# Kernel optimization log

Measured on AMD Instinct MI355X. Metric: run time of the kernel, lower is better.

Reference implementation:

```python
import jax, jax.numpy as jnp
import numpy as np

B, C, L = 4, 16, 1024
U_SELF, U_CROSS, HID = 32, 16, 128
WIDTH = 128
EPS = 1e-5
LN_EPS = 1e-14


def _band_mask(n, w):
    j = jnp.arange(n)
    lo = j - w // 2
    hi = lo + w
    i = j[:, None]
    return (lo <= i) & (i < hi)  # mask[i, j]: query i attends key j


def _layernorm(x, gamma, beta):
    # channel-first LN over dim 1; gamma/beta shape (C, 1)
    mean = jnp.mean(x, 1, keepdims=True)
    var = jnp.mean((x - mean) ** 2, 1, keepdims=True) + LN_EPS
    return (x - mean) / jnp.sqrt(var) * gamma + beta


def _self_attn(x, Wt, Wx, bh, Wa, ba):
    xt = x.transpose(0, 2, 1)                                # (B,L,C)
    q = xt @ Wt                                              # (B,L,U)
    k = xt @ Wx                                              # (B,L,U)
    h = jnp.tanh(q[:, :, None, :] + k[:, None, :, :] + bh)   # (B,L,L,U)
    e = jnp.squeeze(h @ Wa, -1) + ba                         # (B,L,L)
    e = jnp.exp(e - jnp.max(e, -1, keepdims=True))
    e = jnp.where(_band_mask(e.shape[1], WIDTH), e, 0.0)
    a = e / (jnp.sum(e, -1, keepdims=True) + EPS)
    v = a @ xt                                               # (B,L,C)
    return v.transpose(0, 2, 1)


def _ff(x, W1, b1, W2, b2):
    xt = x.transpose(0, 2, 1)
    h = jax.nn.relu(xt @ W1 + b1)
    return (h @ W2 + b2).transpose(0, 2, 1)


def _transformer(x, Wt, Wx, bh, Wa, ba, g1, be1, W1, b1, W2, b2, g2, be2):
    y = _layernorm(x + _self_attn(x, Wt, Wx, bh, Wa, ba), g1, be1)
    return _layernorm(y + _ff(y, W1, b1, W2, b2), g2, be2)


def _cross(y1, y2, Wq, Wk, Wv):
    y1t = y1.transpose(0, 2, 1)
    y2t = y2.transpose(0, 2, 1)
    q = y1t @ Wq
    k = y2t @ Wk
    v = y2t @ Wv                                             # (B,L,Uc)
    e = (q @ k.transpose(0, 2, 1)) * (1.0 / np.float32(np.sqrt(U_CROSS)))
    e = jnp.where(_band_mask(e.shape[-1], WIDTH), e, -jnp.inf)
    a = jax.nn.softmax(e, -1)
    return (a @ v).transpose(0, 2, 1)                        # (B,Uc,L)


def _forward(x1, x2, t1, t2, cw, top):
    y1 = _transformer(x1, *t1)
    y2 = _transformer(x2, *t2)
    g1, be1, W1, b1, W2, b2, g2, be2 = top
    y = _layernorm(y1 + _cross(y1, y2, *cw), g1, be1)
    return _layernorm(y + _ff(y, W1, b1, W2, b2), g2, be2)


def setup_inputs() -> dict:
    key = jax.random.key(0)
    ks = iter(jax.random.split(key, 64))
    u = lambda shape: jax.random.uniform(next(ks), shape, jnp.float32, -0.02, 0.02)
    n = lambda shape: jax.random.normal(next(ks), shape, jnp.float32) * 0.05
    d = {"x1": jax.random.normal(next(ks), (B, C, L), jnp.float32),
         "x2": jax.random.normal(next(ks), (B, C, L), jnp.float32)}
    for p in ("t1", "t2"):
        d[p + "_Wt"] = u((C, U_SELF)); d[p + "_Wx"] = u((C, U_SELF))
        d[p + "_bh"] = jnp.zeros(U_SELF)
        d[p + "_Wa"] = u((U_SELF, 1)); d[p + "_ba"] = jnp.zeros(1)
        d[p + "_g1"] = jnp.ones((C, 1)); d[p + "_be1"] = jnp.zeros((C, 1))
        d[p + "_W1"] = n((C, HID)); d[p + "_b1"] = jnp.zeros(HID)
        d[p + "_W2"] = n((HID, C)); d[p + "_b2"] = jnp.zeros(C)
        d[p + "_g2"] = jnp.ones((C, 1)); d[p + "_be2"] = jnp.zeros((C, 1))
    d["ca_Wq"] = u((C, U_CROSS)); d["ca_Wk"] = u((C, U_CROSS)); d["ca_Wv"] = u((C, U_CROSS))
    d["g1"] = jnp.ones((C, 1)); d["be1"] = jnp.zeros((C, 1))
    d["W1"] = n((C, HID)); d["b1"] = jnp.zeros(HID)
    d["W2"] = n((HID, C)); d["b2"] = jnp.zeros(C)
    d["g2"] = jnp.ones((C, 1)); d["be2"] = jnp.zeros((C, 1))
    return d


def reference(x1, x2, t1_Wt, t1_Wx, t1_bh, t1_Wa, t1_ba, t1_g1, t1_be1, t1_W1, t1_b1, t1_W2, t1_b2, t1_g2, t1_be2, t2_Wt, t2_Wx, t2_bh, t2_Wa, t2_ba, t2_g1, t2_be1, t2_W1, t2_b1, t2_W2, t2_b2, t2_g2, t2_be2, ca_Wq, ca_Wk, ca_Wv, g1, be1, W1, b1, W2, b2, g2, be2):
    t1 = (t1_Wt, t1_Wx, t1_bh, t1_Wa, t1_ba, t1_g1, t1_be1, t1_W1, t1_b1, t1_W2, t1_b2, t1_g2, t1_be2)
    t2 = (t2_Wt, t2_Wx, t2_bh, t2_Wa, t2_ba, t2_g1, t2_be1, t2_W1, t2_b1, t2_W2, t2_b2, t2_g2, t2_be2)
    cw = (ca_Wq, ca_Wk, ca_Wv)
    top = (g1, be1, W1, b1, W2, b2, g2, be2)
    return _forward(x1, x2, t1, t2, cw, top)
```

## Files before the change

### kernel.cpp

```cpp
#include <hip/hip_runtime.h>


#define L_    1024
#define C_    16
#define US_   32
#define HID_  128
#define TI1   8
#define TI2   4
#define K2    2.885390082f
#define L2E   1.442695041f

__device__ __forceinline__ float frcp(float x)  { return __builtin_amdgcn_rcpf(x); }
__device__ __forceinline__ float fexp2(float x) { return __builtin_amdgcn_exp2f(x); }

struct BranchP {
  const float *x, *Wt, *Wx, *bh, *Wa, *ba, *g1, *be1, *W1, *b1, *W2, *b2, *g2, *be2;
  float* y;
};

__global__ __launch_bounds__(256) void branch_kernel(BranchP Pa, BranchP Pb) {
  const BranchP P = blockIdx.z ? Pb : Pa;
  const int b   = blockIdx.y;
  const int i0  = blockIdx.x * TI1;
  const int tid = threadIdx.x;
  const int j0  = max(0, i0 - 63);
  const int j1  = min(L_, i0 + TI1 + 64);
  const int Wd  = j1 - j0;

  __shared__ float xs[C_][137];
  __shared__ union {
    struct { float ks[136][33]; float qs[TI1][33]; } a;
    struct { float W1s[C_][129]; float W2s[HID_][17]; float b1s[HID_]; } bb;
  } ovl;
  __shared__ float es[TI1][129];
  __shared__ float ya[TI1][17];
  __shared__ float Wts[C_][US_], Wxs[C_][US_];
  __shared__ float m2was[US_], bhs[US_];
  __shared__ float g1s[C_], be1s[C_], b2s[C_], g2s[C_], be2s[C_];
  __shared__ float bas;

  float w1r[8], w2r[8], b1r = 0.f;
#pragma unroll
  for (int t = 0; t < 8; ++t) { w1r[t] = P.W1[tid + 256 * t]; w2r[t] = P.W2[tid + 256 * t]; }
  if (tid < HID_) b1r = P.b1[tid];

  for (int idx = tid; idx < C_ * US_; idx += 256) {
    int c = idx >> 5, u = idx & 31;
    Wts[c][u] = K2 * P.Wt[idx];
    Wxs[c][u] = K2 * P.Wx[idx];
  }
  if (tid < US_) { m2was[tid] = -K2 * P.Wa[tid]; bhs[tid] = K2 * P.bh[tid]; }
  if (tid < C_) {
    g1s[tid] = P.g1[tid]; be1s[tid] = P.be1[tid];
    g2s[tid] = P.g2[tid]; be2s[tid] = P.be2[tid];
    b2s[tid] = P.b2[tid];
  }
  if (tid == 0) bas = P.ba[0];
  for (int idx = tid; idx < C_ * Wd; idx += 256) {
    int c = idx / Wd, jj = idx - c * Wd;
    xs[c][jj] = P.x[(b * C_ + c) * L_ + j0 + jj];
  }
  __syncthreads();

  for (int idx = tid; idx < Wd * US_; idx += 256) {
    int j = idx >> 5, u = idx & 31;
    float a = bhs[u];
#pragma unroll
    for (int c = 0; c < C_; ++c) a = fmaf(xs[c][j], Wxs[c][u], a);
    ovl.a.ks[j][u] = a;
  }
  {
    int i = tid >> 5, u = tid & 31;
    float a = 0.f;
#pragma unroll
    for (int c = 0; c < C_; ++c) a = fmaf(xs[c][i0 - j0 + i], Wts[c][u], a);
    ovl.a.qs[i][u] = a;
  }
  __syncthreads();

  const int il   = tid >> 5;
  const int sub  = tid & 31;
  const int ig   = i0 + il;
  const int jlo  = max(0, ig - 63), jhi = min(L_, ig + 65);
  const int nj   = jhi - jlo;
  const int jb   = jlo - j0;
  const int c16  = sub & 15;
  const int half = sub >> 4;

  float inv;
  {
    float xq[US_];
#pragma unroll
    for (int u = 0; u < US_; ++u) xq[u] = ovl.a.qs[il][u];
    float eacc = L2E * bas;
#pragma unroll
    for (int u = 0; u < US_; ++u) eacc -= 0.5f * m2was[u];
    float s = 0.f;
    for (int jj = sub; jj < nj; jj += 32) {
      const float* kr = ovl.a.ks[jb + jj];
      float acc = eacc;
#pragma unroll
      for (int u = 0; u < US_; ++u) {
        float t = fexp2(xq[u] + kr[u]);
        acc = fmaf(m2was[u], frcp(1.0f + t), acc);
      }
      float v = fexp2(acc);
      es[il][jj] = v;
      s += v;
    }
#pragma unroll
    for (int m = 16; m; m >>= 1) s += __shfl_xor(s, m);
    inv = frcp(s + 1e-5f);
  }
  __syncthreads();

#pragma unroll
  for (int t = 0; t < 8; ++t) {
    int idx = tid + 256 * t;
    ovl.bb.W1s[idx >> 7][idx & 127] = w1r[t];
  }
#pragma unroll
  for (int t = 0; t < 8; ++t) {
    int idx = tid + 256 * t;
    ovl.bb.W2s[idx >> 4][idx & 15] = w2r[t];
  }
  if (tid < HID_) ovl.bb.b1s[tid] = b1r;
  float yln;
  {
    float v = 0.f;
    for (int jj = half; jj < nj; jj += 2) v = fmaf(es[il][jj], xs[c16][jb + jj], v);
    v += __shfl_xor(v, 16);
    float y0 = xs[c16][ig - j0] + v * inv;
    float s1 = y0, s2 = y0 * y0;
#pragma unroll
    for (int m = 8; m; m >>= 1) { s1 += __shfl_xor(s1, m); s2 += __shfl_xor(s2, m); }
    float mean = s1 * (1.f / 16.f);
    float var  = s2 * (1.f / 16.f) - mean * mean;
    float rstd = rsqrtf(fmaxf(var, 0.f) + 1e-14f);
    yln = (y0 - mean) * rstd * g1s[c16] + be1s[c16];
    if (half == 0) ya[il][c16] = yln;
  }
  __syncthreads();

#pragma unroll
  for (int t = 0; t < 4; ++t) {
    int u = sub + 32 * t;
    float a = ovl.bb.b1s[u];
#pragma unroll
    for (int c = 0; c < C_; ++c) a = fmaf(ya[il][c], ovl.bb.W1s[c][u], a);
    es[il][u] = fmaxf(a, 0.f);
  }
  __syncthreads();

  {
    float o = 0.f;
    int u0 = half * 64;
#pragma unroll
    for (int uu = 0; uu < 64; ++uu) o = fmaf(es[il][u0 + uu], ovl.bb.W2s[u0 + uu][c16], o);
    o += __shfl_xor(o, 16);
    float y0 = yln + o + b2s[c16];
    float s1 = y0, s2 = y0 * y0;
#pragma unroll
    for (int m = 8; m; m >>= 1) { s1 += __shfl_xor(s1, m); s2 += __shfl_xor(s2, m); }
    float mean = s1 * (1.f / 16.f);
    float var  = s2 * (1.f / 16.f) - mean * mean;
    float rstd = rsqrtf(fmaxf(var, 0.f) + 1e-14f);
    if (half == 0)
      P.y[(b * L_ + ig) * C_ + c16] = (y0 - mean) * rstd * g2s[c16] + be2s[c16];
  }
}

__global__ __launch_bounds__(256) void cross_kernel(
    const float* __restrict__ y1g, const float* __restrict__ y2g,
    const float* Wq, const float* Wk, const float* Wv,
    const float* g1, const float* be1, const float* W1, const float* b1,
    const float* W2, const float* b2, const float* g2, const float* be2,
    float* out) {
  const int b   = blockIdx.y;
  const int i0  = blockIdx.x * TI2;
  const int tid = threadIdx.x;
  const int j0  = max(0, i0 - 63);
  const int j1  = min(L_, i0 + TI2 + 64);
  const int Wd  = j1 - j0;

  __shared__ float y1s[TI2][17];
  __shared__ float y2s[132][17];
  __shared__ float Ms[C_][17];
  __shared__ float zs[TI2][17];
  __shared__ float es[TI2][129];
  __shared__ float ya[TI2][17];
  __shared__ float Wqs[C_][C_], Wks[C_][C_], Wvs[C_][C_];
  __shared__ float W1s[C_][129], W2s[HID_][17], b1s[HID_];
  __shared__ float g1s[C_], be1s[C_], b2s[C_], g2s[C_], be2s[C_];

  {
    int c = tid >> 4, u = tid & 15;
    Wqs[c][u] = Wq[tid]; Wks[c][u] = Wk[tid]; Wvs[c][u] = Wv[tid];
  }
  if (tid < TI2 * C_)
    y1s[tid >> 4][tid & 15] = y1g[(b * L_ + i0 + (tid >> 4)) * C_ + (tid & 15)];
  for (int idx = tid; idx < C_ * HID_; idx += 256) {
    W1s[idx >> 7][idx & 127] = W1[idx];
    W2s[idx >> 4][idx & 15]  = W2[idx];
  }
  if (tid < HID_) b1s[tid] = b1[tid];
  if (tid < C_) {
    g1s[tid] = g1[tid]; be1s[tid] = be1[tid];
    g2s[tid] = g2[tid]; be2s[tid] = be2[tid];
    b2s[tid] = b2[tid];
  }
  for (int idx = tid; idx < Wd * C_; idx += 256) {
    int jj = idx >> 4, c = idx & 15;
    y2s[jj][c] = y2g[(b * L_ + j0 + jj) * C_ + c];
  }
  __syncthreads();

  {
    int c1 = tid >> 4, c2 = tid & 15;
    float m = 0.f;
#pragma unroll
    for (int u = 0; u < C_; ++u) m = fmaf(Wqs[c1][u], Wks[c2][u], m);
    Ms[c1][c2] = (0.25f * L2E) * m;
  }
  __syncthreads();
  if (tid < TI2 * C_) {
    int i = tid >> 4, c = tid & 15;
    float z = 0.f;
#pragma unroll
    for (int cc = 0; cc < C_; ++cc) z = fmaf(y1s[i][cc], Ms[cc][c], z);
    zs[i][c] = z;
  }
  __syncthreads();

  const int il   = tid >> 6;
  const int sub  = tid & 63;
  const int ig   = i0 + il;
  const int jlo  = max(0, ig - 63), jhi = min(L_, ig + 65);
  const int nj   = jhi - jlo;
  const int jb   = jlo - j0;
  const int c16  = sub & 15;
  const int quad = sub >> 4;

  float inv;
  {
    float zr[C_];
#pragma unroll
    for (int c = 0; c < C_; ++c) zr[c] = zs[il][c];
    float s = 0.f;
    for (int jj = sub; jj < nj; jj += 64) {
      const float* yr = y2s[jb + jj];
      float a = 0.f;
#pragma unroll
      for (int c = 0; c < C_; ++c) a = fmaf(zr[c], yr[c], a);
      float v = fexp2(a);
      es[il][jj] = v;
      s += v;
    }
#pragma unroll
    for (int m = 32; m; m >>= 1) s += __shfl_xor(s, m);
    inv = frcp(s);
  }
  __syncthreads();

  {
    float w = 0.f;
    for (int jj = quad; jj < nj; jj += 4) w = fmaf(es[il][jj], y2s[jb + jj][c16], w);
    w += __shfl_xor(w, 16);
    w += __shfl_xor(w, 32);
    if (quad == 0) zs[il][c16] = w * inv;
  }
  __syncthreads();

  float yln;
  {
    float a = 0.f;
#pragma unroll
    for (int c = 0; c < C_; ++c) a = fmaf(zs[il][c], Wvs[c][c16], a);
    float y0 = y1s[il][c16] + a;
    float s1 = y0, s2 = y0 * y0;
#pragma unroll
    for (int m = 8; m; m >>= 1) { s1 += __shfl_xor(s1, m); s2 += __shfl_xor(s2, m); }
    float mean = s1 * (1.f / 16.f);
    float var  = s2 * (1.f / 16.f) - mean * mean;
    float rstd = rsqrtf(fmaxf(var, 0.f) + 1e-14f);
    yln = (y0 - mean) * rstd * g1s[c16] + be1s[c16];
    if (quad == 0) ya[il][c16] = yln;
  }
  __syncthreads();

#pragma unroll
  for (int t = 0; t < 2; ++t) {
    int u = sub + 64 * t;
    float a = b1s[u];
#pragma unroll
    for (int c = 0; c < C_; ++c) a = fmaf(ya[il][c], W1s[c][u], a);
    es[il][u] = fmaxf(a, 0.f);
  }
  __syncthreads();

  {
    float o = 0.f;
    int u0 = quad * 32;
#pragma unroll
    for (int uu = 0; uu < 32; ++uu) o = fmaf(es[il][u0 + uu], W2s[u0 + uu][c16], o);
    o += __shfl_xor(o, 16);
    o += __shfl_xor(o, 32);
    float y0 = yln + o + b2s[c16];
    float s1 = y0, s2 = y0 * y0;
#pragma unroll
    for (int m = 8; m; m >>= 1) { s1 += __shfl_xor(s1, m); s2 += __shfl_xor(s2, m); }
    float mean = s1 * (1.f / 16.f);
    float var  = s2 * (1.f / 16.f) - mean * mean;
    float rstd = rsqrtf(fmaxf(var, 0.f) + 1e-14f);
    if (quad == 0) zs[il][c16] = (y0 - mean) * rstd * g2s[c16] + be2s[c16];
  }
  __syncthreads();

  if (tid < C_ * TI2) {
    int c = tid >> 2, i = tid & 3;
    out[(b * C_ + c) * L_ + i0 + i] = zs[i][c];
  }
}

extern "C" void kernel_launch(void* const* d_in, const int* in_sizes, int n_in,
                              void* d_out, int out_size, void* d_ws, size_t ws_size,
                              hipStream_t stream) {
  (void)in_sizes; (void)n_in; (void)out_size; (void)ws_size;
  const float* const* in = reinterpret_cast<const float* const*>(d_in);
  float* y1w = reinterpret_cast<float*>(d_ws);
  float* y2w = y1w + 4 * L_ * C_;

  BranchP Pa { in[0],  in[2],  in[3],  in[4],  in[5],  in[6],  in[7],
               in[8],  in[9],  in[10], in[11], in[12], in[13], in[14], y1w };
  BranchP Pb { in[1],  in[15], in[16], in[17], in[18], in[19], in[20],
               in[21], in[22], in[23], in[24], in[25], in[26], in[27], y2w };

  branch_kernel<<<dim3(L_ / TI1, 4, 2), 256, 0, stream>>>(Pa, Pb);
  cross_kernel<<<dim3(L_ / TI2, 4), 256, 0, stream>>>(
      y1w, y2w, in[28], in[29], in[30],
      in[31], in[32], in[33], in[34], in[35], in[36], in[37], in[38],
      reinterpret_cast<float*>(d_out));
}
```

Measured before the change: 169.6 us.

## Precompute K/Q projections in separate kernel and read FF weights from global

Adds a kq_kernel that computes the key and query projections once per position for both branches and writes them to workspace. The branch kernel no longer recomputes the overlapping K window per tile. It instead streams K rows from global memory as float4 inside the hot tanh loop and reads Q from shared memory. FF weights W1/W2 are read directly from global/cache instead of being staged in shared memory, in both the branch and cross kernels. This lowers shared memory use, which may raise occupancy, but it adds a kernel launch and global-memory traffic in the innermost loop.

```diff
diff --git a/kernel.cpp b/kernel.cpp
--- a/kernel.cpp
+++ b/kernel.cpp
@@ -13,13 +13,41 @@
 __device__ __forceinline__ float frcp(float x)  { return __builtin_amdgcn_rcpf(x); }
 __device__ __forceinline__ float fexp2(float x) { return __builtin_amdgcn_exp2f(x); }
 
+__global__ __launch_bounds__(256) void kq_kernel(
+    const float* __restrict__ x1, const float* __restrict__ x2,
+    const float* __restrict__ Wt1, const float* __restrict__ Wx1, const float* __restrict__ bh1,
+    const float* __restrict__ Wt2, const float* __restrict__ Wx2, const float* __restrict__ bh2,
+    float* __restrict__ kw, float* __restrict__ qw) {
+  const int idx = blockIdx.x * 256 + threadIdx.x;
+  const int u  = idx & 31;
+  const int j  = (idx >> 5) & 1023;
+  const int b  = (idx >> 15) & 3;
+  const int br = idx >> 17;
+  const float* x  = br ? x2 : x1;
+  const float* Wt = br ? Wt2 : Wt1;
+  const float* Wx = br ? Wx2 : Wx1;
+  const float* bh = br ? bh2 : bh1;
+  float ka = bh[u];
+  float qa = 0.f;
+#pragma unroll
+  for (int c = 0; c < C_; ++c) {
+    float xv = x[(b * C_ + c) * L_ + j];
+    ka = fmaf(xv, Wx[c * US_ + u], ka);
+    qa = fmaf(xv, Wt[c * US_ + u], qa);
+  }
+  kw[idx] = K2 * ka;
+  qw[idx] = K2 * qa;
+}
+
 struct BranchP {
-  const float *x, *Wt, *Wx, *bh, *Wa, *ba, *g1, *be1, *W1, *b1, *W2, *b2, *g2, *be2;
+  const float *x, *Wa, *ba, *g1, *be1, *W1, *b1, *W2, *b2, *g2, *be2;
   float* y;
 };
 
-__global__ __launch_bounds__(256) void branch_kernel(BranchP Pa, BranchP Pb) {
-  const BranchP P = blockIdx.z ? Pb : Pa;
+__global__ __launch_bounds__(256) void branch_kernel(BranchP Pa, BranchP Pb,
+    const float* __restrict__ kw, const float* __restrict__ qw) {
+  const int br  = blockIdx.z;
+  const BranchP P = br ? Pb : Pa;
   const int b   = blockIdx.y;
   const int i0  = blockIdx.x * TI1;
   const int tid = threadIdx.x;
@@ -28,28 +56,20 @@
   const int Wd  = j1 - j0;
 
   __shared__ float xs[C_][137];
-  __shared__ union {
-    struct { float ks[136][33]; float qs[TI1][33]; } a;
-    struct { float W1s[C_][129]; float W2s[HID_][17]; float b1s[HID_]; } bb;
-  } ovl;
+  __shared__ float qs[TI1][33];
   __shared__ float es[TI1][129];
   __shared__ float ya[TI1][17];
-  __shared__ float Wts[C_][US_], Wxs[C_][US_];
-  __shared__ float m2was[US_], bhs[US_];
+  __shared__ float m2was[US_];
+  __shared__ float b1s[HID_];
   __shared__ float g1s[C_], be1s[C_], b2s[C_], g2s[C_], be2s[C_];
   __shared__ float bas;
 
-  float w1r[8], w2r[8], b1r = 0.f;
-#pragma unroll
-  for (int t = 0; t < 8; ++t) { w1r[t] = P.W1[tid + 256 * t]; w2r[t] = P.W2[tid + 256 * t]; }
-  if (tid < HID_) b1r = P.b1[tid];
-
-  for (int idx = tid; idx < C_ * US_; idx += 256) {
-    int c = idx >> 5, u = idx & 31;
-    Wts[c][u] = K2 * P.Wt[idx];
-    Wxs[c][u] = K2 * P.Wx[idx];
-  }
-  if (tid < US_) { m2was[tid] = -K2 * P.Wa[tid]; bhs[tid] = K2 * P.bh[tid]; }
+  {
+    int row = tid >> 5, u = tid & 31;
+    qs[row][u] = qw[(((br * 4 + b) << 10) + i0 + row) * US_ + u];
+  }
+  if (tid < US_) m2was[tid] = -K2 * P.Wa[tid];
+  if (tid < HID_) b1s[tid] = P.b1[tid];
   if (tid < C_) {
     g1s[tid] = P.g1[tid]; be1s[tid] = P.be1[tid];
     g2s[tid] = P.g2[tid]; be2s[tid] = P.be2[tid];
@@ -59,22 +79,6 @@
   for (int idx = tid; idx < C_ * Wd; idx += 256) {
     int c = idx / Wd, jj = idx - c * Wd;
     xs[c][jj] = P.x[(b * C_ + c) * L_ + j0 + jj];
-  }
-  __syncthreads();
-
-  for (int idx = tid; idx < Wd * US_; idx += 256) {
-    int j = idx >> 5, u = idx & 31;
-    float a = bhs[u];
-#pragma unroll
-    for (int c = 0; c < C_; ++c) a = fmaf(xs[c][j], Wxs[c][u], a);
-    ovl.a.ks[j][u] = a;
-  }
-  {
-    int i = tid >> 5, u = tid & 31;
-    float a = 0.f;
-#pragma unroll
-    for (int c = 0; c < C_; ++c) a = fmaf(xs[c][i0 - j0 + i], Wts[c][u], a);
-    ovl.a.qs[i][u] = a;
   }
   __syncthreads();
 
@@ -89,20 +93,22 @@
 
   float inv;
   {
-    float xq[US_];
-#pragma unroll
-    for (int u = 0; u < US_; ++u) xq[u] = ovl.a.qs[il][u];
     float eacc = L2E * bas;
 #pragma unroll
     for (int u = 0; u < US_; ++u) eacc -= 0.5f * m2was[u];
+    const float4* kbase =
+        reinterpret_cast<const float4*>(kw + ((((br * 4 + b) << 10) + jlo) * US_));
     float s = 0.f;
     for (int jj = sub; jj < nj; jj += 32) {
-      const float* kr = ovl.a.ks[jb + jj];
+      const float4* kr = kbase + jj * 8;
       float acc = eacc;
 #pragma unroll
-      for (int u = 0; u < US_; ++u) {
-        float t = fexp2(xq[u] + kr[u]);
-        acc = fmaf(m2was[u], frcp(1.0f + t), acc);
+      for (int t = 0; t < 8; ++t) {
+        float4 kv = kr[t];
+        acc = fmaf(m2was[4*t+0], frcp(1.f + fexp2(qs[il][4*t+0] + kv.x)), acc);
+        acc = fmaf(m2was[4*t+1], frcp(1.f + fexp2(qs[il][4*t+1] + kv.y)), acc);
+        acc = fmaf(m2was[4*t+2], frcp(1.f + fexp2(qs[il][4*t+2] + kv.z)), acc);
+        acc = fmaf(m2was[4*t+3], frcp(1.f + fexp2(qs[il][4*t+3] + kv.w)), acc);
       }
       float v = fexp2(acc);
       es[il][jj] = v;
@@ -114,17 +120,6 @@
   }
   __syncthreads();
 
-#pragma unroll
-  for (int t = 0; t < 8; ++t) {
-    int idx = tid + 256 * t;
-    ovl.bb.W1s[idx >> 7][idx & 127] = w1r[t];
-  }
-#pragma unroll
-  for (int t = 0; t < 8; ++t) {
-    int idx = tid + 256 * t;
-    ovl.bb.W2s[idx >> 4][idx & 15] = w2r[t];
-  }
-  if (tid < HID_) ovl.bb.b1s[tid] = b1r;
   float yln;
   {
     float v = 0.f;
@@ -145,9 +140,9 @@
 #pragma unroll
   for (int t = 0; t < 4; ++t) {
     int u = sub + 32 * t;
-    float a = ovl.bb.b1s[u];
-#pragma unroll
-    for (int c = 0; c < C_; ++c) a = fmaf(ya[il][c], ovl.bb.W1s[c][u], a);
+    float a = b1s[u];
+#pragma unroll
+    for (int c = 0; c < C_; ++c) a = fmaf(ya[il][c], P.W1[c * HID_ + u], a);
     es[il][u] = fmaxf(a, 0.f);
   }
   __syncthreads();
@@ -156,7 +151,8 @@
     float o = 0.f;
     int u0 = half * 64;
 #pragma unroll
-    for (int uu = 0; uu < 64; ++uu) o = fmaf(es[il][u0 + uu], ovl.bb.W2s[u0 + uu][c16], o);
+    for (int uu = 0; uu < 64; ++uu)
+      o = fmaf(es[il][u0 + uu], P.W2[(u0 + uu) * C_ + c16], o);
     o += __shfl_xor(o, 16);
     float y0 = yln + o + b2s[c16];
     float s1 = y0, s2 = y0 * y0;
@@ -173,8 +169,8 @@
 __global__ __launch_bounds__(256) void cross_kernel(
     const float* __restrict__ y1g, const float* __restrict__ y2g,
     const float* Wq, const float* Wk, const float* Wv,
-    const float* g1, const float* be1, const float* W1, const float* b1,
-    const float* W2, const float* b2, const float* g2, const float* be2,
+    const float* g1, const float* be1, const float* __restrict__ W1, const float* b1,
+    const float* __restrict__ W2, const float* b2, const float* g2, const float* be2,
     float* out) {
   const int b   = blockIdx.y;
   const int i0  = blockIdx.x * TI2;
@@ -190,7 +186,7 @@
   __shared__ float es[TI2][129];
   __shared__ float ya[TI2][17];
   __shared__ float Wqs[C_][C_], Wks[C_][C_], Wvs[C_][C_];
-  __shared__ float W1s[C_][129], W2s[HID_][17], b1s[HID_];
+  __shared__ float b1s[HID_];
   __shared__ float g1s[C_], be1s[C_], b2s[C_], g2s[C_], be2s[C_];
 
   {
@@ -199,10 +195,6 @@
   }
   if (tid < TI2 * C_)
     y1s[tid >> 4][tid & 15] = y1g[(b * L_ + i0 + (tid >> 4)) * C_ + (tid & 15)];
-  for (int idx = tid; idx < C_ * HID_; idx += 256) {
-    W1s[idx >> 7][idx & 127] = W1[idx];
-    W2s[idx >> 4][idx & 15]  = W2[idx];
-  }
   if (tid < HID_) b1s[tid] = b1[tid];
   if (tid < C_) {
     g1s[tid] = g1[tid]; be1s[tid] = be1[tid];
@@ -293,7 +285,7 @@
     int u = sub + 64 * t;
     float a = b1s[u];
 #pragma unroll
-    for (int c = 0; c < C_; ++c) a = fmaf(ya[il][c], W1s[c][u], a);
+    for (int c = 0; c < C_; ++c) a = fmaf(ya[il][c], W1[c * HID_ + u], a);
     es[il][u] = fmaxf(a, 0.f);
   }
   __syncthreads();
@@ -302,7 +294,8 @@
     float o = 0.f;
     int u0 = quad * 32;
 #pragma unroll
-    for (int uu = 0; uu < 32; ++uu) o = fmaf(es[il][u0 + uu], W2s[u0 + uu][c16], o);
+    for (int uu = 0; uu < 32; ++uu)
+      o = fmaf(es[il][u0 + uu], W2[(u0 + uu) * C_ + c16], o);
     o += __shfl_xor(o, 16);
     o += __shfl_xor(o, 32);
     float y0 = yln + o + b2s[c16];
@@ -329,13 +322,18 @@
   const float* const* in = reinterpret_cast<const float* const*>(d_in);
   float* y1w = reinterpret_cast<float*>(d_ws);
   float* y2w = y1w + 4 * L_ * C_;
-
-  BranchP Pa { in[0],  in[2],  in[3],  in[4],  in[5],  in[6],  in[7],
-               in[8],  in[9],  in[10], in[11], in[12], in[13], in[14], y1w };
-  BranchP Pb { in[1],  in[15], in[16], in[17], in[18], in[19], in[20],
-               in[21], in[22], in[23], in[24], in[25], in[26], in[27], y2w };
-
-  branch_kernel<<<dim3(L_ / TI1, 4, 2), 256, 0, stream>>>(Pa, Pb);
+  float* kw  = y2w + 4 * L_ * C_;
+  float* qw  = kw + 2 * 4 * L_ * US_;
+
+  kq_kernel<<<1024, 256, 0, stream>>>(
+      in[0], in[1], in[2], in[3], in[4], in[15], in[16], in[17], kw, qw);
+
+  BranchP Pa { in[0],  in[5],  in[6],  in[7],  in[8],
+               in[9],  in[10], in[11], in[12], in[13], in[14], y1w };
+  BranchP Pb { in[1],  in[18], in[19], in[20], in[21],
+               in[22], in[23], in[24], in[25], in[26], in[27], y2w };
+
+  branch_kernel<<<dim3(L_ / TI1, 4, 2), 256, 0, stream>>>(Pa, Pb, kw, qw);
   cross_kernel<<<dim3(L_ / TI2, 4), 256, 0, stream>>>(
       y1w, y2w, in[28], in[29], in[30],
       in[31], in[32], in[33], in[34], in[35], in[36], in[37], in[38],
```

Result: no change. 168.5 us (-0.7%).
